# Kernel tuning notes

Measured on AMD Instinct MI355X. Metric: run time of the kernel, lower is better.

Reference implementation:

```python
import jax, jax.numpy as jnp
import numpy as np

W_SIZE = 7
K = 15
EPS = 1e-8  # torch cosine_similarity eps


def setup_inputs() -> dict:
    key = jax.random.key(0)
    k0, k1, k2 = jax.random.split(key, 3)
    dim = 128
    return {
        "x_in": jax.random.normal(k0, (4, dim, 112, 112), dtype=jnp.float32),
        "f_w": jax.random.normal(k1, (dim // 8, dim), dtype=jnp.float32) * (1.0 / np.sqrt(dim)),
        "f_b": jax.random.normal(k2, (dim // 8,), dtype=jnp.float32) * 0.01,
        "edge_alpha": jnp.ones((1,), dtype=jnp.float32),
        "edge_beta": jnp.zeros((1,), dtype=jnp.float32),
    }


def reference(x_in, f_w, f_b, edge_alpha, edge_beta):
    B, C, H, W = x_in.shape
    Wg = Hg = W_SIZE
    w, h = H // Wg, W // Hg
    N = w * h
    # patchify: b c (Wg w) (Hg h) -> (b Wg Hg) c w h
    xp = x_in.reshape(B, C, Wg, w, Hg, h).transpose(0, 2, 4, 1, 3, 5).reshape(B * Wg * Hg, C, w, h)
    P = xp.shape[0]
    # 1x1 conv f: C -> C//8 channels
    f = jnp.einsum('pcwh,dc->pdwh', xp, f_w) + f_b[None, :, None, None]
    Cf = f.shape[1]
    x_flat = f.reshape(P, Cf, N).transpose(0, 2, 1)  # [P, N, Cf]
    # normalized spatial grid (torch std is unbiased -> ddof=1)
    gi, gj = jnp.meshgrid(jnp.arange(w, dtype=jnp.float32), jnp.arange(h, dtype=jnp.float32), indexing='ij')
    grid = jnp.stack([gi, gj], axis=-1).reshape(N, 2)
    grid = (grid - grid.mean(0)) / (grid.std(0, ddof=1) + 1e-5)
    x_aug = jnp.concatenate([x_flat, jnp.broadcast_to(grid[None], (P, N, 2))], axis=-1)  # [P,N,Cf+2]
    # pairwise cosine similarity via normalized dot products
    nrm = jnp.maximum(jnp.linalg.norm(x_aug, axis=-1, keepdims=True), EPS)
    xn = x_aug / nrm
    sim = jnp.einsum('pnd,pmd->pnm', xn, xn)  # [P,N,N]
    topv, topi = jax.lax.top_k(sim, K)        # [P,N,K]
    # edge weights; scatter_softmax over row index == softmax over k (each row has exactly K edges)
    weights = jax.nn.sigmoid(edge_beta[0] + edge_alpha[0] * topv)
    wn = jax.nn.softmax(weights, axis=-1)     # [P,N,K]
    # gather original-channel messages from top-k neighbors and aggregate
    xo = xp.reshape(P, C, N).transpose(0, 2, 1)                 # [P,N,C]
    gathered = jax.vmap(lambda xr, ir: xr[ir])(xo, topi)        # [P,N,K,C]
    out_flat = jnp.einsum('pnk,pnkc->pnc', wn, gathered)        # [P,N,C]
    out = out_flat.reshape(P, w, h, C).transpose(0, 3, 1, 2)    # [P,C,w,h]
    # un-patchify: (b Wg Hg) c w h -> b c (Wg w) (Hg h)
    out = out.reshape(B, Wg, Hg, C, w, h).transpose(0, 3, 1, 4, 2, 5).reshape(B, C, H, W)
    return out
```

## Files before the change

kernel.cpp:

```cpp
#include <hip/hip_runtime.h>
#include <math.h>

#define KSEL 15
#define CIN 128
#define CF 16
#define HH 112
#define PLANE 12544
#define NN 256
#define ROWSTRIDE 20
#define KVSTRIDE 260

static __device__ __forceinline__ unsigned mono32(float f) {
    unsigned u = __float_as_uint(f);
    return ((int)u < 0) ? ~u : (u | 0x80000000u);
}
static __device__ __forceinline__ float demono32(unsigned u) {
    return ((int)u < 0) ? __uint_as_float(u & 0x7FFFFFFFu) : __uint_as_float(~u);
}

__global__ __launch_bounds__(256) void k1_features(
    const float* __restrict__ x, const float* __restrict__ fw, const float* __restrict__ fb,
    double* __restrict__ xa64, float* __restrict__ xa32, unsigned* __restrict__ dirtyCount)
{
    __shared__ float lfw[CIN * CF];
    __shared__ float lfb[CF];
    const int tid = threadIdx.x;
    if (blockIdx.x == 0 && tid == 0) *dirtyCount = 0u;
    const int p  = blockIdx.x >> 2;
    const int n0 = (blockIdx.x & 3) * 64;
    const int b = p / 49, g = p % 49;
    const int gI = g / 7, gJ = g % 7;
    const float* xb = x + (size_t)b * CIN * PLANE + (size_t)(gI * 16 * HH + gJ * 16);

    for (int q = tid; q < CIN * CF; q += 256) { int d = q >> 7, c = q & 127; lfw[c * CF + d] = fw[q]; }
    if (tid < CF) lfb[tid] = fb[tid];
    __syncthreads();

    const int nl = tid >> 2, dq = tid & 3;
    const int n = n0 + nl, i = n >> 4, j = n & 15;
    const float* xp = xb + i * HH + j;

    double e0 = 0.0, e1 = 0.0, e2 = 0.0, e3 = 0.0;
    double o0 = 0.0, o1 = 0.0, o2 = 0.0, o3 = 0.0;
#pragma unroll 2
    for (int c = 0; c < CIN; c += 2) {
        double xc0 = (double)xp[(size_t)c * PLANE];
        double xc1 = (double)xp[(size_t)(c + 1) * PLANE];
        float4 wv0 = *(const float4*)&lfw[c * CF + dq * 4];
        float4 wv1 = *(const float4*)&lfw[(c + 1) * CF + dq * 4];
        e0 = fma(xc0, (double)wv0.x, e0);
        e1 = fma(xc0, (double)wv0.y, e1);
        e2 = fma(xc0, (double)wv0.z, e2);
        e3 = fma(xc0, (double)wv0.w, e3);
        o0 = fma(xc1, (double)wv1.x, o0);
        o1 = fma(xc1, (double)wv1.y, o1);
        o2 = fma(xc1, (double)wv1.z, o2);
        o3 = fma(xc1, (double)wv1.w, o3);
    }
    double a0 = e0 + o0 + (double)lfb[dq * 4 + 0];
    double a1 = e1 + o1 + (double)lfb[dq * 4 + 1];
    double a2 = e2 + o2 + (double)lfb[dq * 4 + 2];
    double a3 = e3 + o3 + (double)lfb[dq * 4 + 3];

    const double GDIV = 4.618802153517006 + 1e-5;
    double gx = ((double)i - 7.5) / GDIV;
    double gy = ((double)j - 7.5) / GDIV;

    double ss = a0 * a0;
    ss = fma(a1, a1, ss); ss = fma(a2, a2, ss); ss = fma(a3, a3, ss);
    if (dq == 3) { ss = fma(gx, gx, ss); ss = fma(gy, gy, ss); }
    ss += __shfl_xor(ss, 1);
    ss += __shfl_xor(ss, 2);
    double nrm = fmax(sqrt(ss), 1e-8);

    size_t ro = ((size_t)p * NN + n) * ROWSTRIDE;
    double f0 = a0 / nrm, f1 = a1 / nrm, f2 = a2 / nrm, f3 = a3 / nrm;
    xa64[ro + dq * 4 + 0] = f0; xa64[ro + dq * 4 + 1] = f1;
    xa64[ro + dq * 4 + 2] = f2; xa64[ro + dq * 4 + 3] = f3;
    xa32[ro + dq * 4 + 0] = (float)f0; xa32[ro + dq * 4 + 1] = (float)f1;
    xa32[ro + dq * 4 + 2] = (float)f2; xa32[ro + dq * 4 + 3] = (float)f3;
    if (dq == 3) {
        double g0 = gx / nrm, g1 = gy / nrm;
        xa64[ro + 16] = g0; xa64[ro + 17] = g1; xa64[ro + 18] = 0.0; xa64[ro + 19] = 0.0;
        xa32[ro + 16] = (float)g0; xa32[ro + 17] = (float)g1; xa32[ro + 18] = 0.f; xa32[ro + 19] = 0.f;
    }
}

__global__ __launch_bounds__(256) void k2_select(
    const float* __restrict__ xa32,
    const float* __restrict__ ea, const float* __restrict__ eb,
    int* __restrict__ topi, float* __restrict__ wkout,
    unsigned* __restrict__ dirtyCount, int* __restrict__ dirtyList)
{
    __shared__ float tile[NN * ROWSTRIDE];
    __shared__ unsigned kv[16 * KVSTRIDE];
    const int tid = threadIdx.x;
    const int p = blockIdx.x >> 4, sub = blockIdx.x & 15;

    const float* src = xa32 + (size_t)p * NN * ROWSTRIDE;
#pragma unroll
    for (int q = 0; q < 5; ++q) {
        int idx = q * 256 + tid;
        ((float4*)tile)[idx] = ((const float4*)src)[idx];
    }
    __syncthreads();

    const int w    = tid >> 6;
    const int lane = tid & 63;
    const int r0   = sub * 16 + w * 4;
    const int m0   = lane * 4;

    float xr[4][18];
#pragma unroll
    for (int rr = 0; rr < 4; ++rr) {
        const float4* xp4 = (const float4*)&tile[(r0 + rr) * ROWSTRIDE];
        float4 x0 = xp4[0], x1 = xp4[1], x2 = xp4[2], x3 = xp4[3];
        float2 xt = *(const float2*)&tile[(r0 + rr) * ROWSTRIDE + 16];
        xr[rr][0]=x0.x; xr[rr][1]=x0.y; xr[rr][2]=x0.z; xr[rr][3]=x0.w;
        xr[rr][4]=x1.x; xr[rr][5]=x1.y; xr[rr][6]=x1.z; xr[rr][7]=x1.w;
        xr[rr][8]=x2.x; xr[rr][9]=x2.y; xr[rr][10]=x2.z; xr[rr][11]=x2.w;
        xr[rr][12]=x3.x; xr[rr][13]=x3.y; xr[rr][14]=x3.z; xr[rr][15]=x3.w;
        xr[rr][16]=xt.x; xr[rr][17]=xt.y;
    }

    unsigned keys[4][4];
#pragma unroll
    for (int mm = 0; mm < 4; ++mm) {
        const int m = m0 + mm;
        const float4* bp4 = (const float4*)&tile[m * ROWSTRIDE];
        float4 b0 = bp4[0], b1 = bp4[1], b2 = bp4[2], b3 = bp4[3];
        float2 bt = *(const float2*)&tile[m * ROWSTRIDE + 16];
#pragma unroll
        for (int rr = 0; rr < 4; ++rr) {
            float s = 0.f;
            s = fmaf(xr[rr][0],  b0.x, s); s = fmaf(xr[rr][1],  b0.y, s);
            s = fmaf(xr[rr][2],  b0.z, s); s = fmaf(xr[rr][3],  b0.w, s);
            s = fmaf(xr[rr][4],  b1.x, s); s = fmaf(xr[rr][5],  b1.y, s);
            s = fmaf(xr[rr][6],  b1.z, s); s = fmaf(xr[rr][7],  b1.w, s);
            s = fmaf(xr[rr][8],  b2.x, s); s = fmaf(xr[rr][9],  b2.y, s);
            s = fmaf(xr[rr][10], b2.z, s); s = fmaf(xr[rr][11], b2.w, s);
            s = fmaf(xr[rr][12], b3.x, s); s = fmaf(xr[rr][13], b3.y, s);
            s = fmaf(xr[rr][14], b3.z, s); s = fmaf(xr[rr][15], b3.w, s);
            s = fmaf(xr[rr][16], bt.x, s); s = fmaf(xr[rr][17], bt.y, s);
            keys[rr][mm] = (mono32(s) & 0xFFFFFF00u) | (unsigned)(255 - m);
        }
    }
#pragma unroll
    for (int rr = 0; rr < 4; ++rr) {
        uint4 kw = make_uint4(keys[rr][0], keys[rr][1], keys[rr][2], keys[rr][3]);
        *(uint4*)&kv[(w * 4 + rr) * KVSTRIDE + m0] = kw;
    }
    __syncthreads();

    const int l16 = tid & 15;
    const int rb  = tid >> 4;
    const int row = p * NN + sub * 16 + rb;

    unsigned k[16];
    {
        const uint4* kp = (const uint4*)&kv[rb * KVSTRIDE + l16 * 16];
        uint4 q0 = kp[0], q1 = kp[1], q2 = kp[2], q3 = kp[3];
        k[0]=q0.x; k[1]=q0.y; k[2]=q0.z; k[3]=q0.w;
        k[4]=q1.x; k[5]=q1.y; k[6]=q1.z; k[7]=q1.w;
        k[8]=q2.x; k[9]=q2.y; k[10]=q2.z; k[11]=q2.w;
        k[12]=q3.x; k[13]=q3.y; k[14]=q3.z; k[15]=q3.w;
    }

#pragma unroll
    for (int kk = 2; kk <= 16; kk <<= 1) {
#pragma unroll
        for (int jj = kk >> 1; jj > 0; jj >>= 1) {
#pragma unroll
            for (int ii = 0; ii < 16; ++ii) {
                int ll = ii ^ jj;
                if (ll > ii) {
                    bool up = ((ii & kk) == 0);
                    unsigned a = k[ii], bbv = k[ll];
                    bool sw = up ? (a > bbv) : (a < bbv);
                    k[ii] = sw ? bbv : a; k[ll] = sw ? a : bbv;
                }
            }
        }
    }

    int ptr = 15;
    unsigned myhead = k[15];
    unsigned mycand = 0;
#pragma unroll
    for (int e = 0; e < 16; ++e) {
        unsigned W = myhead;
        unsigned o;
        o = __shfl_xor(W, 1);  W = (o > W) ? o : W;
        o = __shfl_xor(W, 2);  W = (o > W) ? o : W;
        o = __shfl_xor(W, 4);  W = (o > W) ? o : W;
        o = __shfl_xor(W, 8);  W = (o > W) ? o : W;
        if (l16 == e) mycand = W;
        bool won = (myhead == W);
        ptr -= won ? 1 : 0;
        int rp = ptr < 0 ? 0 : ptr;
        unsigned nh = k[0];
#pragma unroll
        for (int ii = 1; ii < 16; ++ii) nh = (rp == ii) ? k[ii] : nh;
        myhead = won ? nh : myhead;
    }

    unsigned v15 = __shfl(mycand, 14, 16);
    unsigned v16 = __shfl(mycand, 15, 16);
    float lo = demono32(v15 & 0xFFFFFF00u) - 1e-5f;
    float hi = demono32((v16 & 0xFFFFFF00u) + 0x100u) + 1e-5f;
    bool dirty = !(hi < lo);
    if (l16 == 0 && dirty) {
        unsigned slot = atomicAdd(dirtyCount, 1u);
        dirtyList[slot] = row;
    }

    int mym = 255 - (int)(mycand & 0xFFu);
    float sv = demono32(mycand & 0xFFFFFF00u);
    float alpha = ea[0], beta = eb[0];
    float sg = 1.f / (1.f + expf(-(beta + alpha * sv)));
    float v = (l16 < KSEL) ? sg : -1e30f;
    float mx = v, of;
    of = __shfl_xor(mx, 1); mx = fmaxf(mx, of);
    of = __shfl_xor(mx, 2); mx = fmaxf(mx, of);
    of = __shfl_xor(mx, 4); mx = fmaxf(mx, of);
    of = __shfl_xor(mx, 8); mx = fmaxf(mx, of);
    float ex = expf(v - mx);
    float sm = ex;
    of = __shfl_xor(sm, 1); sm += of;
    of = __shfl_xor(sm, 2); sm += of;
    of = __shfl_xor(sm, 4); sm += of;
    of = __shfl_xor(sm, 8); sm += of;

    topi[row * 16 + l16] = mym;
    wkout[row * 16 + l16] = (l16 < KSEL) ? (ex / sm) : 0.f;
}

__global__ __launch_bounds__(64) void k2b_dirty(
    const double* __restrict__ xa64, const float* __restrict__ ea, const float* __restrict__ eb,
    const unsigned* __restrict__ dirtyCount, const int* __restrict__ dirtyList,
    int* __restrict__ topi, float* __restrict__ wkout)
{
    const int nd = (int)*dirtyCount;
    const int lane = threadIdx.x;
    for (int idx = blockIdx.x; idx < nd; idx += gridDim.x) {
        const int row = dirtyList[idx];
        const int p = row >> 8;
        const double* xr64 = xa64 + (size_t)row * ROWSTRIDE;

        double sv[4]; int smi[4];
#pragma unroll
        for (int s4 = 0; s4 < 4; ++s4) {
            int m = s4 * 64 + lane;
            const double* xm64 = xa64 + ((size_t)p * NN + m) * ROWSTRIDE;
            double s = 0.0;
#pragma unroll
            for (int d = 0; d < 18; ++d) s = fma(xr64[d], xm64[d], s);
            sv[s4] = s; smi[s4] = m;
        }

        double cv = -3.0; int cm = 0;
#pragma unroll
        for (int e = 0; e < KSEL; ++e) {
            double lv = sv[0]; int lm = smi[0];
#pragma unroll
            for (int s4 = 1; s4 < 4; ++s4) {
                bool t = (sv[s4] > lv) || (sv[s4] == lv && smi[s4] < lm);
                lv = t ? sv[s4] : lv; lm = t ? smi[s4] : lm;
            }
#pragma unroll
            for (int off = 1; off < 64; off <<= 1) {
                double ov = __shfl_xor(lv, off);
                int    om = __shfl_xor(lm, off);
                bool t = (ov > lv) || (ov == lv && om < lm);
                lv = t ? ov : lv; lm = t ? om : lm;
            }
            if (lane == e) { cv = lv; cm = lm; }
#pragma unroll
            for (int s4 = 0; s4 < 4; ++s4) if (smi[s4] == lm) sv[s4] = -3.0;
        }

        float alpha = ea[0], beta = eb[0];
        float sg = 1.f / (1.f + expf(-(beta + alpha * (float)cv)));
        float v = (lane < KSEL) ? sg : -1e30f;
        float mx = v, of;
        for (int off = 1; off < 64; off <<= 1) { of = __shfl_xor(mx, off); mx = fmaxf(mx, of); }
        float ex = expf(v - mx);
        float sm = ex;
        for (int off = 1; off < 64; off <<= 1) { of = __shfl_xor(sm, off); sm += of; }
        float w = ex / sm;
        if (lane < 16) {
            topi[row * 16 + lane] = (lane < KSEL) ? cm : 0;
            wkout[row * 16 + lane] = (lane < KSEL) ? w : 0.f;
        }
    }
}

__global__ __launch_bounds__(256) void k3_aggregate(
    const float* __restrict__ x, const int* __restrict__ topi, const float* __restrict__ wk,
    float* __restrict__ out)
{
    __shared__ float tile[NN * ROWSTRIDE];
    const int tid = threadIdx.x;
    const int pb = blockIdx.x >> 3, cg = blockIdx.x & 7, c0 = cg * 16;
    const int b = pb / 49, g = pb % 49;
    const int gI = g / 7, gJ = g % 7;
    const float* xb = x + ((size_t)b * CIN + c0) * PLANE + (size_t)(gI * 16 * HH + gJ * 16);

#pragma unroll
    for (int rep = 0; rep < 4; ++rep) {
        int linear = rep * 256 + tid;
        int cc = linear >> 6, chunk = linear & 63;
        int pos = chunk * 4, ii = pos >> 4, jj = pos & 15;
        float4 v = *(const float4*)(xb + (size_t)cc * PLANE + ii * HH + jj);
        tile[(pos + 0) * ROWSTRIDE + cc] = v.x;
        tile[(pos + 1) * ROWSTRIDE + cc] = v.y;
        tile[(pos + 2) * ROWSTRIDE + cc] = v.z;
        tile[(pos + 3) * ROWSTRIDE + cc] = v.w;
    }
    __syncthreads();

    const int n = tid;
    const int row = pb * NN + n;
    float acc[16];
#pragma unroll
    for (int c = 0; c < 16; ++c) acc[c] = 0.f;

#pragma unroll
    for (int kq = 0; kq < 4; ++kq) {
        int4   mi4 = ((const int4*)(topi + (size_t)row * 16))[kq];
        float4 w4  = ((const float4*)(wk  + (size_t)row * 16))[kq];
        const int   mis[4] = { mi4.x, mi4.y, mi4.z, mi4.w };
        const float ws4[4] = { w4.x, w4.y, w4.z, w4.w };
#pragma unroll
        for (int u = 0; u < 4; ++u) {
            float w = ws4[u];
            const float4* sp = (const float4*)&tile[mis[u] * ROWSTRIDE];
#pragma unroll
            for (int q = 0; q < 4; ++q) {
                float4 f = sp[q];
                acc[q * 4 + 0] = fmaf(w, f.x, acc[q * 4 + 0]);
                acc[q * 4 + 1] = fmaf(w, f.y, acc[q * 4 + 1]);
                acc[q * 4 + 2] = fmaf(w, f.z, acc[q * 4 + 2]);
                acc[q * 4 + 3] = fmaf(w, f.w, acc[q * 4 + 3]);
            }
        }
    }
    const int ii = n >> 4, jj = n & 15;
    float* ob = out + ((size_t)b * CIN + c0) * PLANE + (size_t)(gI * 16 * HH + gJ * 16) + ii * HH + jj;
#pragma unroll
    for (int cc = 0; cc < 16; ++cc) ob[(size_t)cc * PLANE] = acc[cc];
}

extern "C" void kernel_launch(void* const* d_in, const int* in_sizes, int n_in,
                              void* d_out, int out_size, void* d_ws, size_t ws_size,
                              hipStream_t stream) {
    const float* x  = (const float*)d_in[0];
    const float* fw = (const float*)d_in[1];
    const float* fb = (const float*)d_in[2];
    const float* ea = (const float*)d_in[3];
    const float* eb = (const float*)d_in[4];
    float* out = (float*)d_out;

    int nB = in_sizes[0] / (CIN * PLANE);
    int nP = nB * 49;
    size_t nRows = (size_t)nP * NN;

    char* wsb = (char*)d_ws;
    size_t off = 0;
    auto carve = [&](size_t bytes) { char* r = wsb + off; off = (off + bytes + 255) & ~(size_t)255; return r; };
    double*   xa64   = (double*)  carve(nRows * ROWSTRIDE * sizeof(double));
    float*    xa32   = (float*)   carve(nRows * ROWSTRIDE * sizeof(float));
    int*      topi   = (int*)     carve(nRows * 16 * sizeof(int));
    float*    wk     = (float*)   carve(nRows * 16 * sizeof(float));
    unsigned* dcnt   = (unsigned*)carve(256);
    int*      dlist  = (int*)     carve(nRows * sizeof(int));

    hipLaunchKernelGGL(k1_features, dim3(nP * 4), dim3(256), 0, stream, x, fw, fb, xa64, xa32, dcnt);
    hipLaunchKernelGGL(k2_select,   dim3(nP * 16), dim3(256), 0, stream, xa32, ea, eb, topi, wk, dcnt, dlist);
    hipLaunchKernelGGL(k2b_dirty,   dim3(256), dim3(64), 0, stream, xa64, ea, eb, dcnt, dlist, topi, wk);
    hipLaunchKernelGGL(k3_aggregate, dim3(nP * 8), dim3(256), 0, stream, x, topi, wk, out);
}
```

Before: 173.2 us.

## Transpose feature tile for similarity and cut register pressure in top-k merge

```diff
diff --git a/kernel.cpp b/kernel.cpp
--- a/kernel.cpp
+++ b/kernel.cpp
@@ -8,7 +8,7 @@
 #define PLANE 12544
 #define NN 256
 #define ROWSTRIDE 20
-#define KVSTRIDE 260
+#define KVROW 272
 
 static __device__ __forceinline__ unsigned mono32(float f) {
     unsigned u = __float_as_uint(f);
@@ -20,7 +20,8 @@
 
 __global__ __launch_bounds__(256) void k1_features(
     const float* __restrict__ x, const float* __restrict__ fw, const float* __restrict__ fb,
-    double* __restrict__ xa64, float* __restrict__ xa32, unsigned* __restrict__ dirtyCount)
+    double* __restrict__ xa64, float* __restrict__ xa32, float* __restrict__ xa32T,
+    unsigned* __restrict__ dirtyCount)
 {
     __shared__ float lfw[CIN * CF];
     __shared__ float lfb[CF];
@@ -79,43 +80,54 @@
     xa64[ro + dq * 4 + 2] = f2; xa64[ro + dq * 4 + 3] = f3;
     xa32[ro + dq * 4 + 0] = (float)f0; xa32[ro + dq * 4 + 1] = (float)f1;
     xa32[ro + dq * 4 + 2] = (float)f2; xa32[ro + dq * 4 + 3] = (float)f3;
+    size_t tb = ((size_t)p * 18 + dq * 4) * NN + n;
+    xa32T[tb + 0 * NN] = (float)f0;
+    xa32T[tb + 1 * NN] = (float)f1;
+    xa32T[tb + 2 * NN] = (float)f2;
+    xa32T[tb + 3 * NN] = (float)f3;
     if (dq == 3) {
         double g0 = gx / nrm, g1 = gy / nrm;
         xa64[ro + 16] = g0; xa64[ro + 17] = g1; xa64[ro + 18] = 0.0; xa64[ro + 19] = 0.0;
         xa32[ro + 16] = (float)g0; xa32[ro + 17] = (float)g1; xa32[ro + 18] = 0.f; xa32[ro + 19] = 0.f;
+        size_t tg = ((size_t)p * 18 + 16) * NN + n;
+        xa32T[tg] = (float)g0; xa32T[tg + NN] = (float)g1;
     }
 }
 
 __global__ __launch_bounds__(256) void k2_select(
-    const float* __restrict__ xa32,
+    const float* __restrict__ xa32, const float* __restrict__ xa32T,
     const float* __restrict__ ea, const float* __restrict__ eb,
     int* __restrict__ topi, float* __restrict__ wkout,
     unsigned* __restrict__ dirtyCount, int* __restrict__ dirtyList)
 {
-    __shared__ float tile[NN * ROWSTRIDE];
-    __shared__ unsigned kv[16 * KVSTRIDE];
+    __shared__ float tileT[18 * NN];
+    __shared__ float rowTile[16 * ROWSTRIDE];
+    __shared__ unsigned kv[16 * KVROW];
     const int tid = threadIdx.x;
     const int p = blockIdx.x >> 4, sub = blockIdx.x & 15;
 
-    const float* src = xa32 + (size_t)p * NN * ROWSTRIDE;
-#pragma unroll
-    for (int q = 0; q < 5; ++q) {
-        int idx = q * 256 + tid;
-        ((float4*)tile)[idx] = ((const float4*)src)[idx];
+    const float4* srcT = (const float4*)(xa32T + (size_t)p * 18 * NN);
+    for (int q = tid; q < (18 * NN / 4); q += 256)
+        ((float4*)tileT)[q] = srcT[q];
+    if (tid < (16 * ROWSTRIDE / 4)) {
+        const float4* srcR = (const float4*)(xa32 + ((size_t)p * NN + sub * 16) * ROWSTRIDE);
+        ((float4*)rowTile)[tid] = srcR[tid];
     }
     __syncthreads();
 
     const int w    = tid >> 6;
     const int lane = tid & 63;
-    const int r0   = sub * 16 + w * 4;
     const int m0   = lane * 4;
 
     float xr[4][18];
 #pragma unroll
     for (int rr = 0; rr < 4; ++rr) {
-        const float4* xp4 = (const float4*)&tile[(r0 + rr) * ROWSTRIDE];
-        float4 x0 = xp4[0], x1 = xp4[1], x2 = xp4[2], x3 = xp4[3];
-        float2 xt = *(const float2*)&tile[(r0 + rr) * ROWSTRIDE + 16];
+        const float* rp_ = &rowTile[(w * 4 + rr) * ROWSTRIDE];
+        float4 x0 = *(const float4*)&rp_[0];
+        float4 x1 = *(const float4*)&rp_[4];
+        float4 x2 = *(const float4*)&rp_[8];
+        float4 x3 = *(const float4*)&rp_[12];
+        float2 xt = *(const float2*)&rp_[16];
         xr[rr][0]=x0.x; xr[rr][1]=x0.y; xr[rr][2]=x0.z; xr[rr][3]=x0.w;
         xr[rr][4]=x1.x; xr[rr][5]=x1.y; xr[rr][6]=x1.z; xr[rr][7]=x1.w;
         xr[rr][8]=x2.x; xr[rr][9]=x2.y; xr[rr][10]=x2.z; xr[rr][11]=x2.w;
@@ -123,48 +135,39 @@
         xr[rr][16]=xt.x; xr[rr][17]=xt.y;
     }
 
-    unsigned keys[4][4];
-#pragma unroll
-    for (int mm = 0; mm < 4; ++mm) {
-        const int m = m0 + mm;
-        const float4* bp4 = (const float4*)&tile[m * ROWSTRIDE];
-        float4 b0 = bp4[0], b1 = bp4[1], b2 = bp4[2], b3 = bp4[3];
-        float2 bt = *(const float2*)&tile[m * ROWSTRIDE + 16];
+    float s0[4], s1[4], s2[4], s3[4];
+#pragma unroll
+    for (int rr = 0; rr < 4; ++rr) { s0[rr]=0.f; s1[rr]=0.f; s2[rr]=0.f; s3[rr]=0.f; }
+#pragma unroll 6
+    for (int d = 0; d < 18; ++d) {
+        float4 bd = *(const float4*)&tileT[d * NN + m0];
 #pragma unroll
         for (int rr = 0; rr < 4; ++rr) {
-            float s = 0.f;
-            s = fmaf(xr[rr][0],  b0.x, s); s = fmaf(xr[rr][1],  b0.y, s);
-            s = fmaf(xr[rr][2],  b0.z, s); s = fmaf(xr[rr][3],  b0.w, s);
-            s = fmaf(xr[rr][4],  b1.x, s); s = fmaf(xr[rr][5],  b1.y, s);
-            s = fmaf(xr[rr][6],  b1.z, s); s = fmaf(xr[rr][7],  b1.w, s);
-            s = fmaf(xr[rr][8],  b2.x, s); s = fmaf(xr[rr][9],  b2.y, s);
-            s = fmaf(xr[rr][10], b2.z, s); s = fmaf(xr[rr][11], b2.w, s);
-            s = fmaf(xr[rr][12], b3.x, s); s = fmaf(xr[rr][13], b3.y, s);
-            s = fmaf(xr[rr][14], b3.z, s); s = fmaf(xr[rr][15], b3.w, s);
-            s = fmaf(xr[rr][16], bt.x, s); s = fmaf(xr[rr][17], bt.y, s);
-            keys[rr][mm] = (mono32(s) & 0xFFFFFF00u) | (unsigned)(255 - m);
+            float a = xr[rr][d];
+            s0[rr] = fmaf(a, bd.x, s0[rr]);
+            s1[rr] = fmaf(a, bd.y, s1[rr]);
+            s2[rr] = fmaf(a, bd.z, s2[rr]);
+            s3[rr] = fmaf(a, bd.w, s3[rr]);
         }
     }
 #pragma unroll
     for (int rr = 0; rr < 4; ++rr) {
-        uint4 kw = make_uint4(keys[rr][0], keys[rr][1], keys[rr][2], keys[rr][3]);
-        *(uint4*)&kv[(w * 4 + rr) * KVSTRIDE + m0] = kw;
+        unsigned k0 = (mono32(s0[rr]) & 0xFFFFFF00u) | (unsigned)(255 - (m0 + 0));
+        unsigned k1 = (mono32(s1[rr]) & 0xFFFFFF00u) | (unsigned)(255 - (m0 + 1));
+        unsigned k2 = (mono32(s2[rr]) & 0xFFFFFF00u) | (unsigned)(255 - (m0 + 2));
+        unsigned k3 = (mono32(s3[rr]) & 0xFFFFFF00u) | (unsigned)(255 - (m0 + 3));
+        *(uint4*)&kv[(w * 4 + rr) * KVROW + m0] = make_uint4(k0, k1, k2, k3);
     }
     __syncthreads();
 
     const int l16 = tid & 15;
     const int rb  = tid >> 4;
     const int row = p * NN + sub * 16 + rb;
+    const int kvb = rb * KVROW + l16;
 
     unsigned k[16];
-    {
-        const uint4* kp = (const uint4*)&kv[rb * KVSTRIDE + l16 * 16];
-        uint4 q0 = kp[0], q1 = kp[1], q2 = kp[2], q3 = kp[3];
-        k[0]=q0.x; k[1]=q0.y; k[2]=q0.z; k[3]=q0.w;
-        k[4]=q1.x; k[5]=q1.y; k[6]=q1.z; k[7]=q1.w;
-        k[8]=q2.x; k[9]=q2.y; k[10]=q2.z; k[11]=q2.w;
-        k[12]=q3.x; k[13]=q3.y; k[14]=q3.z; k[15]=q3.w;
-    }
+#pragma unroll
+    for (int s = 0; s < 16; ++s) k[s] = kv[kvb + 16 * s];
 
 #pragma unroll
     for (int kk = 2; kk <= 16; kk <<= 1) {
@@ -175,33 +178,39 @@
                 int ll = ii ^ jj;
                 if (ll > ii) {
                     bool up = ((ii & kk) == 0);
-                    unsigned a = k[ii], bbv = k[ll];
-                    bool sw = up ? (a > bbv) : (a < bbv);
-                    k[ii] = sw ? bbv : a; k[ll] = sw ? a : bbv;
+                    unsigned a = k[ii], bv = k[ll];
+                    bool sw = up ? (a > bv) : (a < bv);
+                    k[ii] = sw ? bv : a; k[ll] = sw ? a : bv;
                 }
             }
         }
     }
-
+#pragma unroll
+    for (int s = 0; s < 16; ++s) kv[kvb + 16 * s] = k[s];
+
+    unsigned h14 = k[14], h13 = k[13], h12 = k[12], h11 = k[11];
     int ptr = 15;
     unsigned myhead = k[15];
     unsigned mycand = 0;
 #pragma unroll
     for (int e = 0; e < 16; ++e) {
-        unsigned W = myhead;
-        unsigned o;
+        unsigned W = myhead, o;
         o = __shfl_xor(W, 1);  W = (o > W) ? o : W;
         o = __shfl_xor(W, 2);  W = (o > W) ? o : W;
         o = __shfl_xor(W, 4);  W = (o > W) ? o : W;
         o = __shfl_xor(W, 8);  W = (o > W) ? o : W;
         if (l16 == e) mycand = W;
         bool won = (myhead == W);
-        ptr -= won ? 1 : 0;
-        int rp = ptr < 0 ? 0 : ptr;
-        unsigned nh = k[0];
-#pragma unroll
-        for (int ii = 1; ii < 16; ++ii) nh = (rp == ii) ? k[ii] : nh;
-        myhead = won ? nh : myhead;
+        if (won) {
+            ptr--;
+            int rp = ptr < 0 ? 0 : ptr;
+            unsigned nh = h14;
+            nh = (rp == 13) ? h13 : nh;
+            nh = (rp == 12) ? h12 : nh;
+            nh = (rp == 11) ? h11 : nh;
+            if (rp <= 10) nh = kv[kvb + 16 * rp];
+            myhead = nh;
+        }
     }
 
     unsigned v15 = __shfl(mycand, 14, 16);
@@ -370,13 +379,14 @@
     auto carve = [&](size_t bytes) { char* r = wsb + off; off = (off + bytes + 255) & ~(size_t)255; return r; };
     double*   xa64   = (double*)  carve(nRows * ROWSTRIDE * sizeof(double));
     float*    xa32   = (float*)   carve(nRows * ROWSTRIDE * sizeof(float));
+    float*    xa32T  = (float*)   carve((size_t)nP * 18 * NN * sizeof(float));
     int*      topi   = (int*)     carve(nRows * 16 * sizeof(int));
     float*    wk     = (float*)   carve(nRows * 16 * sizeof(float));
     unsigned* dcnt   = (unsigned*)carve(256);
     int*      dlist  = (int*)     carve(nRows * sizeof(int));
 
-    hipLaunchKernelGGL(k1_features, dim3(nP * 4), dim3(256), 0, stream, x, fw, fb, xa64, xa32, dcnt);
-    hipLaunchKernelGGL(k2_select,   dim3(nP * 16), dim3(256), 0, stream, xa32, ea, eb, topi, wk, dcnt, dlist);
+    hipLaunchKernelGGL(k1_features, dim3(nP * 4), dim3(256), 0, stream, x, fw, fb, xa64, xa32, xa32T, dcnt);
+    hipLaunchKernelGGL(k2_select,   dim3(nP * 16), dim3(256), 0, stream, xa32, xa32T, ea, eb, topi, wk, dcnt, dlist);
     hipLaunchKernelGGL(k2b_dirty,   dim3(256), dim3(64), 0, stream, xa64, ea, eb, dcnt, dlist, topi, wk);
     hipLaunchKernelGGL(k3_aggregate, dim3(nP * 8), dim3(256), 0, stream, x, topi, wk, out);
 }
```

After: 209.9 us. +21.2%, slower.
